# Kernel tuning notes

Hardware: AMD Instinct MI355X
Metric: run time of the kernel (lower is better)

The kernel has to match this reference:

```python
import jax, jax.numpy as jnp
import numpy as np
from jax import lax

SEQ_LEN, PRED_LEN, C_IN, D_MODEL, KS = 96, 48, 7, 128, 5
PAD = (KS - 1) // 2


def setup_inputs() -> dict:
    key = jax.random.key(0)
    ks = jax.random.split(key, 20)
    B = 512
    s = 0.02
    inp = {
        "x_enc": jax.random.normal(ks[0], (B, SEQ_LEN, C_IN), jnp.float32),
        "x_mark": jax.random.randint(ks[1], (B, SEQ_LEN, 4), 0, 7),
        "y_mark": jax.random.randint(ks[2], (B, SEQ_LEN + PRED_LEN, 4), 0, 7),
        # temporal embedding tables
        "hour_emb": jax.random.normal(ks[3], (24, D_MODEL)) * s,
        "weekday_emb": jax.random.normal(ks[4], (7, D_MODEL)) * s,
        "day_emb": jax.random.normal(ks[5], (32, D_MODEL)) * s,
        "month_emb": jax.random.normal(ks[6], (13, D_MODEL)) * s,
        # value embedding Linear(C_IN -> D_MODEL)
        "W_val": jax.random.normal(ks[7], (D_MODEL, C_IN)) * s,
        "b_val": jnp.zeros((D_MODEL,)),
        # three Conv1d(D_MODEL, D_MODEL, KS)
        "conv1_w": jax.random.normal(ks[8], (D_MODEL, D_MODEL, KS)) * s,
        "conv1_b": jnp.zeros((D_MODEL,)),
        "conv2_w": jax.random.normal(ks[9], (D_MODEL, D_MODEL, KS)) * s,
        "conv2_b": jnp.zeros((D_MODEL,)),
        "conv3_w": jax.random.normal(ks[10], (D_MODEL, D_MODEL, KS)) * s,
        "conv3_b": jnp.zeros((D_MODEL,)),
        # GRU (PyTorch layout: 3*D rows ordered [r, z, n])
        "gru_Wi": jax.random.normal(ks[11], (3 * D_MODEL, D_MODEL)) * s,
        "gru_Wh": jax.random.normal(ks[12], (3 * D_MODEL, D_MODEL)) * s,
        "gru_bi": jnp.zeros((3 * D_MODEL,)),
        "gru_bh": jnp.zeros((3 * D_MODEL,)),
        # fc Linear(D_MODEL -> C_IN)
        "fc_w": jax.random.normal(ks[13], (C_IN, D_MODEL)) * s,
        "fc_b": jnp.zeros((C_IN,)),
    }
    return inp


def _conv1d(x, w, b):
    # x: [B, D, T], w: [O, I, K]
    y = lax.conv_general_dilated(x, w, window_strides=(1,), padding=[(PAD, PAD)],
                                 dimension_numbers=("NCH", "OIH", "NCH"))
    return y + b[None, :, None]


def _gru_last(x, Wi, Wh, bi, bh):
    # x: [B, T, D] -> final hidden state [B, D] (PyTorch GRU equations)
    B, T, D = x.shape
    gx = jnp.einsum("btd,gd->btg", x, Wi) + bi  # [B, T, 3D]
    h0 = jnp.zeros((B, D), x.dtype)

    def step(h, gxt):
        gh = h @ Wh.T + bh
        r = jax.nn.sigmoid(gxt[:, :D] + gh[:, :D])
        z = jax.nn.sigmoid(gxt[:, D:2 * D] + gh[:, D:2 * D])
        n = jnp.tanh(gxt[:, 2 * D:] + r * gh[:, 2 * D:])
        return (1.0 - z) * n + z * h, None

    h_last, _ = lax.scan(step, h0, jnp.swapaxes(gx, 0, 1))
    return h_last


def reference(x_enc, x_mark, y_mark,
              hour_emb, weekday_emb, day_emb, month_emb,
              W_val, b_val,
              conv1_w, conv1_b, conv2_w, conv2_b, conv3_w, conv3_b,
              gru_Wi, gru_Wh, gru_bi, gru_bh, fc_w, fc_b):
    B = x_enc.shape[0]
    # temporal embedding for the full y_mark window (pointwise; precompute once)
    temb = (hour_emb[y_mark[:, :, 0]] + weekday_emb[y_mark[:, :, 1]]
            + day_emb[y_mark[:, :, 2]] + month_emb[y_mark[:, :, 3]])  # [B, L, D]

    x_cat = jnp.concatenate([x_enc, jnp.zeros((B, PRED_LEN, C_IN), x_enc.dtype)], axis=1)

    def one_step(x_cat, i):
        xw = lax.dynamic_slice(x_cat, (0, i, 0), (B, SEQ_LEN, C_IN))
        tw = lax.dynamic_slice(temb, (0, i, 0), (B, SEQ_LEN, D_MODEL))
        x = jnp.einsum("btc,dc->btd", xw, W_val) + b_val + tw  # [B, T, D]
        x = jnp.swapaxes(x, 1, 2)  # [B, D, T]
        x = jax.nn.relu(_conv1d(x, conv1_w, conv1_b))
        x = jax.nn.relu(_conv1d(x, conv2_w, conv2_b))
        x = jax.nn.relu(_conv1d(x, conv3_w, conv3_b))
        x = jnp.swapaxes(x, 1, 2)  # [B, T, D]
        h = _gru_last(x, gru_Wi, gru_Wh, gru_bi, gru_bh)  # [B, D]
        pred = h @ fc_w.T + fc_b  # [B, C]
        x_cat = lax.dynamic_update_slice(x_cat, pred[:, None, :], (0, SEQ_LEN + i, 0))
        return x_cat, None

    x_cat, _ = lax.scan(one_step, x_cat, jnp.arange(PRED_LEN))
    return x_cat[:, -PRED_LEN:, :]
```

## Files before the change

kernel.cpp:

```cpp
#include <hip/hip_runtime.h>

#define B_SZ 512
#define SEQ 96
#define PRED 48
#define TOT 144
#define CIN 7
#define DM 128
#define GDIM 384
#define KS 5

#define CSTR 132
#define ASUB (20*CSTR)
#define WROW 136
#define SWZ(o) ((o) + ((((o) >> 6)) << 2))

#define W_CONV (KS*DM*DM)
#define OFF_WIT (3*W_CONV)
#define OFF_WHT (3*W_CONV + DM*GDIM)
#define W_TOTAL (3*W_CONV + 2*DM*GDIM)

#define NBB 2

__device__ float g_gxg[(size_t)B_SZ*TOT*GDIM];
__device__ float g_gxe[B_SZ*12*GDIM];
__device__ float g_wT[W_TOTAL];

__global__ void prep_weights(const float* __restrict__ w1, const float* __restrict__ w2,
                             const float* __restrict__ w3, const float* __restrict__ Wi,
                             const float* __restrict__ Wh) {
    int tid = blockIdx.x*256 + threadIdx.x;
    if (tid < 3*W_CONV) {
        int l = tid / W_CONV, r = tid % W_CONV;
        int o = r & 127, c = (r >> 7) & 127, k = r >> 14;
        const float* w = (l==0) ? w1 : ((l==1) ? w2 : w3);
        g_wT[tid] = w[o*(DM*KS) + c*KS + k];
    } else if (tid < W_TOTAL) {
        int r = tid - 3*W_CONV;
        int m = r / (DM*GDIM), q = r % (DM*GDIM);
        int g = q % GDIM, c = q / GDIM;
        const float* W = (m==0) ? Wi : Wh;
        g_wT[tid] = W[g*DM + c];
    }
}

template<int NJ>
__device__ __forceinline__ void fma8(float (&acc)[NJ][8], int j, float a,
                                     const float4& wA, const float4& wB) {
    acc[j][0] = fmaf(a, wA.x, acc[j][0]);
    acc[j][1] = fmaf(a, wA.y, acc[j][1]);
    acc[j][2] = fmaf(a, wA.z, acc[j][2]);
    acc[j][3] = fmaf(a, wA.w, acc[j][3]);
    acc[j][4] = fmaf(a, wB.x, acc[j][4]);
    acc[j][5] = fmaf(a, wB.y, acc[j][5]);
    acc[j][6] = fmaf(a, wB.z, acc[j][6]);
    acc[j][7] = fmaf(a, wB.w, acc[j][7]);
}

__device__ __forceinline__ void stage_conv_chunk(float* __restrict__ wbuf,
                                                 const float* __restrict__ wT,
                                                 int cc, int tid) {
    const int cj = tid >> 5, oo = (tid & 31) * 4;
    #pragma unroll
    for (int k = 0; k < KS; ++k)
        *(float4*)(wbuf + (k*8 + cj)*WROW + SWZ(oo)) =
            *(const float4*)(wT + (k*DM + cc*8 + cj)*DM + oo);
}

template<int NJ>
__device__ __forceinline__ void conv_layer_chunked(float* __restrict__ buf,
                                                   float* __restrict__ wbuf,
                                                   const float* __restrict__ wT,
                                                   const float* __restrict__ bias,
                                                   int nrow, int winO, int tid) {
    const int og = tid & 15, ttg = tid >> 4;
    const int o0 = og*8, so0 = SWZ(o0), r0 = ttg*NJ;
    const bool act = (r0 < nrow);
    float acc[NJ][8];
// ... 82 lines not shown
    const float* WiT = g_wT + OFF_WIT;
    float ga[3][24];
    #pragma unroll
    for (int e = 0; e < 24; ++e) {
        float bv = gbi[g0+e];
        #pragma unroll
        for (int j = 0; j < 3; ++j) ga[j][e] = bv;
    }
    for (int cc = 0; cc < DM/8; ++cc) {
        __syncthreads();
        #pragma unroll
        for (int s = 0; s < 3; ++s)
            ((float4*)wbuf)[s*256 + tid] = ((const float4*)(WiT + cc*8*GDIM))[s*256 + tid];
        __syncthreads();
        const int c0 = cc*8;
        #pragma unroll
        for (int cj = 0; cj < 8; cj += 2) {
            float2 a2[3];
            #pragma unroll
            for (int m = 0; m < 3; ++m)
                a2[m] = *(const float2*)(buf + (r0+m)*CSTR + c0 + cj);
            float4 w4[6];
            #pragma unroll
            for (int q = 0; q < 6; ++q)
                w4[q] = *(const float4*)(wbuf + cj*GDIM + g0 + q*4);
            const float* wv = (const float*)w4;
            #pragma unroll
            for (int j = 0; j < 3; ++j)
                #pragma unroll
                for (int e = 0; e < 24; ++e)
                    ga[j][e] = fmaf(a2[j].x, wv[e], ga[j][e]);
            #pragma unroll
            for (int q = 0; q < 6; ++q)
                w4[q] = *(const float4*)(wbuf + (cj+1)*GDIM + g0 + q*4);
            #pragma unroll
            for (int j = 0; j < 3; ++j)
                #pragma unroll
                for (int e = 0; e < 24; ++e)
                    ga[j][e] = fmaf(a2[j].y, wv[e], ga[j][e]);
        }
    }
    #pragma unroll
    for (int j = 0; j < 3; ++j) {
        int w = cs + r0 + j;
        if (w >= 6 && w < 90) {
            float* gxo = g_gxg + ((size_t)b*TOT + w)*GDIM + g0;
            #pragma unroll
            for (int q = 0; q < 6; ++q)
                *(float4*)(gxo + q*4) = *(const float4*)&ga[j][q*4];
        }
    }
}

template<int NJ>
__device__ __forceinline__ void mlayer(float* __restrict__ abuf, float* __restrict__ wbuf,
                                       const float* __restrict__ wT,
                                       const float* __restrict__ bias,
                                       int R, int off, int tid) {
    const int og = tid & 15, ttg = tid >> 4;
    const int o0 = og*8, so0 = SWZ(o0);
    const int m0 = ttg * NJ;
    const bool act = (m0 < 2*R);
    int s = 0, r0 = 0;
    if (act) { s = m0 / R; r0 = m0 - s*R; }
    float* in = abuf + s*ASUB;
    float acc[NJ][8];
    #pragma unroll
    for (int u = 0; u < 8; ++u) {
        float bv = bias[o0+u];
        #pragma unroll
        for (int j = 0; j < NJ; ++j) acc[j][u] = bv;
    }
    for (int cc = 0; cc < DM/8; ++cc) {
        __syncthreads();
        stage_conv_chunk(wbuf, wT, cc, tid);
        __syncthreads();
        if (act) {
            const int c0 = cc*8;
            #pragma unroll
            for (int cj = 0; cj < 8; cj += 2) {
                float2 a2[NJ+4];
                #pragma unroll
                for (int m = 0; m < NJ+4; ++m)
                    a2[m] = *(const float2*)(in + (r0+m)*CSTR + c0 + cj);
                #pragma unroll
                for (int k = 0; k < KS; ++k) {
                    const float4 wA0 = *(const float4*)(wbuf + (k*8+cj)*WROW + so0);
                    const float4 wB0 = *(const float4*)(wbuf + (k*8+cj)*WROW + so0 + 4);
                    const float4 wA1 = *(const float4*)(wbuf + (k*8+cj+1)*WROW + so0);
                    const float4 wB1 = *(const float4*)(wbuf + (k*8+cj+1)*WROW + so0 + 4);
                    #pragma unroll
                    for (int j = 0; j < NJ; ++j) {
                        fma8(acc, j, a2[j+k].x, wA0, wB0);
                        fma8(acc, j, a2[j+k].y, wA1, wB1);
                    }
                }
            }
        }
    }
    __syncthreads();
    if (act) {
        const int wb = s ? 83 : -6;
        #pragma unroll
        for (int j = 0; j < NJ; ++j) {
            int q = r0 + j, w = wb + off + q;
            bool valid = (w >= 0) && (w < SEQ);
            #pragma unroll
            for (int u = 0; u < 8; ++u)
                in[q*CSTR + o0+u] = valid ? fmaxf(acc[j][u], 0.f) : 0.f;
        }
    }
    __syncthreads();
}

__launch_bounds__(256, 3)
__global__ void step_kernel(int i, const float* __restrict__ x_enc,
                            const int* __restrict__ y_mark,
                            const float* __restrict__ hour_e, const float* __restrict__ wk_e,
                            const float* __restrict__ day_e, const float* __restrict__ mon_e,
                            const float* __restrict__ W_val, const float* __restrict__ b_val,
                            const float* __restrict__ b1, const float* __restrict__ b2,
                            const float* __restrict__ b3, const float* __restrict__ gbi,
                            const float* __restrict__ out) {
    __shared__ float abuf[2*ASUB];
    __shared__ float wbuf[16*GDIM];
    const int tid = threadIdx.x;
    const int b = blockIdx.x;

    for (int e = tid; e < 2*20*DM; e += 256) {
        int s = e / (20*DM);
        int rem = e - s*(20*DM);
        int q = rem >> 7, d = rem & 127;
        int wb = s ? 83 : -6;
        int w = wb + q;
        float v = 0.f;
        if (w >= 0 && w < SEQ) {
            int p = i + w;
            const float* xr = (p < SEQ) ? (x_enc + (b*SEQ + p)*CIN)
                                        : (out + (b*PRED + (p - SEQ))*CIN);
            v = b_val[d];
            #pragma unroll
            for (int c = 0; c < CIN; ++c) v = fmaf(xr[c], W_val[d*CIN + c], v);
            const int* ym = y_mark + (b*TOT + p)*4;
            v += hour_e[ym[0]*DM + d] + wk_e[ym[1]*DM + d]
               + day_e[ym[2]*DM + d] + mon_e[ym[3]*DM + d];
        }
        abuf[s*ASUB + q*CSTR + d] = v;
    }
    mlayer<2>(abuf, wbuf, g_wT,            b1, 16, 2, tid);
    mlayer<2>(abuf, wbuf, g_wT + W_CONV,   b2, 12, 4, tid);
    mlayer<1>(abuf, wbuf, g_wT + 2*W_CONV, b3,  8, 6, tid);

    const int mp = tid >> 5;
    const int g0 = (tid & 31) * 12;
    const int s = mp >> 2;
    const int row0 = (2*mp) & 7;
    const float* a0p = abuf + s*ASUB + row0*CSTR;
    const float* a1p = a0p + CSTR;
    const float* WiT = g_wT + OFF_WIT;
    float ga[2][12];
    #pragma unroll
    for (int e = 0; e < 12; ++e) { float bv = gbi[g0+e]; ga[0][e] = bv; ga[1][e] = bv; }
    for (int cc = 0; cc < 8; ++cc) {
        __syncthreads();
        for (int x = tid; x < 16*GDIM/4; x += 256)
            ((float4*)wbuf)[x] = ((const float4*)(WiT + cc*16*GDIM))[x];
        __syncthreads();
        #pragma unroll
        for (int c = 0; c < 16; ++c) {
            float av0 = a0p[cc*16 + c];
            float av1 = a1p[cc*16 + c];
            const float* wr = wbuf + c*GDIM + g0;
            #pragma unroll
            for (int q4 = 0; q4 < 3; ++q4) {
                float4 w4 = *(const float4*)(wr + q4*4);
                ga[0][q4*4+0] = fmaf(av0, w4.x, ga[0][q4*4+0]);
                ga[0][q4*4+1] = fmaf(av0, w4.y, ga[0][q4*4+1]);
                ga[0][q4*4+2] = fmaf(av0, w4.z, ga[0][q4*4+2]);
                ga[0][q4*4+3] = fmaf(av0, w4.w, ga[0][q4*4+3]);
                ga[1][q4*4+0] = fmaf(av1, w4.x, ga[1][q4*4+0]);
                ga[1][q4*4+1] = fmaf(av1, w4.y, ga[1][q4*4+1]);
                ga[1][q4*4+2] = fmaf(av1, w4.z, ga[1][q4*4+2]);
                ga[1][q4*4+3] = fmaf(av1, w4.w, ga[1][q4*4+3]);
            }
        }
    }
    const int wb = s ? 83 : -6;
    #pragma unroll
    for (int j = 0; j < 2; ++j) {
        int w = wb + 6 + row0 + j;
        float* dst = nullptr;
        if (s == 0) {
            if (w < 6) dst = g_gxe + ((size_t)b*12 + w)*GDIM + g0;
        } else {
            if (w == 89)      dst = g_gxg + ((size_t)b*TOT + (i + 89))*GDIM + g0;
            else if (w < SEQ) dst = g_gxe + ((size_t)b*12 + (w - 84))*GDIM + g0;
        }
        if (dst) {
            *(float4*)(dst)     = *(const float4*)&ga[j][0];
            *(float4*)(dst + 4) = *(const float4*)&ga[j][4];
            *(float4*)(dst + 8) = *(const float4*)&ga[j][8];
        }
    }
}

__launch_bounds__(512, 2)
__global__ void gru_rec(int i, const float* __restrict__ gbh,
                        const float* __restrict__ fc_w, const float* __restrict__ fc_b,
                        float* __restrict__ out) {
    __shared__ __align__(16) float H[2][NBB][DM];
    __shared__ float P[3][4][NBB][DM];
    const int tid = threadIdx.x;
    const int j = tid & 127, s = tid >> 7;
    const int b0 = blockIdx.x * NBB;

    float whr[32], whz[32], whn[32];
    {
        const float* Wp = g_wT + OFF_WHT + (size_t)(32*s)*GDIM + j;
        #pragma unroll
        for (int c = 0; c < 32; ++c) {
            whr[c] = Wp[c*GDIM];
            whz[c] = Wp[c*GDIM + DM];
            whn[c] = Wp[c*GDIM + 2*DM];
        }
    }

    const int cb = s & 1, cj = j;
    const bool comb = (tid < NBB*DM);
    float bhr = 0.f, bhz = 0.f, bhn = 0.f;
    if (comb) {
        bhr = gbh[cj]; bhz = gbh[DM + cj]; bhn = gbh[2*DM + cj];
        H[0][cb][cj] = 0.f;
    }

    const float* gxg_b0 = g_gxg + (size_t)(b0)*TOT*GDIM;
    const float* gxe_b0 = g_gxe + (size_t)(b0)*12*GDIM;
    auto gp = [&](int t, int bb) -> const float* {
        return (t < 6)  ? (gxe_b0 + (size_t)bb*12*GDIM + t*GDIM)
             : (t < 90) ? (gxg_b0 + (size_t)bb*TOT*GDIM + (size_t)(i + t)*GDIM)
                        : (gxe_b0 + (size_t)bb*12*GDIM + (t - 84)*GDIM);
    };

    float gxr = 0.f, gxz = 0.f, gxn = 0.f;
    if (comb) {
        const float* g0p = gp(0, cb);
        gxr = g0p[cj]; gxz = g0p[DM + cj]; gxn = g0p[2*DM + cj];
    }
    __syncthreads();

    for (int t = 0; t < SEQ; ++t) {
        #pragma unroll
        for (int b = 0; b < NBB; ++b) {
            const float* Hc = &H[t & 1][b][32*s];
            float ar = 0.f, az = 0.f, an = 0.f;
            #pragma unroll
            for (int c = 0; c < 32; c += 4) {
                float4 h4 = *(const float4*)(Hc + c);
                ar = fmaf(h4.x, whr[c],   ar); az = fmaf(h4.x, whz[c],   az); an = fmaf(h4.x, whn[c],   an);
                ar = fmaf(h4.y, whr[c+1], ar); az = fmaf(h4.y, whz[c+1], az); an = fmaf(h4.y, whn[c+1], an);
                ar = fmaf(h4.z, whr[c+2], ar); az = fmaf(h4.z, whz[c+2], az); an = fmaf(h4.z, whn[c+2], an);
                ar = fmaf(h4.w, whr[c+3], ar); az = fmaf(h4.w, whz[c+3], az); an = fmaf(h4.w, whn[c+3], an);
            }
            P[0][s][b][j] = ar;
            P[1][s][b][j] = az;
            P[2][s][b][j] = an;
        }
        __syncthreads();
        if (comb) {
            float ar = bhr + ((P[0][0][cb][cj] + P[0][1][cb][cj]) + (P[0][2][cb][cj] + P[0][3][cb][cj]));
            float az = bhz + ((P[1][0][cb][cj] + P[1][1][cb][cj]) + (P[1][2][cb][cj] + P[1][3][cb][cj]));
            float an = bhn + ((P[2][0][cb][cj] + P[2][1][cb][cj]) + (P[2][2][cb][cj] + P[2][3][cb][cj]));
            float r = 1.f/(1.f + __expf(-(gxr + ar)));
            float z = 1.f/(1.f + __expf(-(gxz + az)));
            float xn = gxn + r*an;
            float e2 = __expf(2.f*xn);
            float n = 1.f - 2.f/(e2 + 1.f);
            float h = (1.f - z)*n + z*H[t & 1][cb][cj];
            H[(t + 1) & 1][cb][cj] = h;
            if (t + 1 < SEQ) {
                const float* gq = gp(t + 1, cb);
                gxr = gq[cj]; gxz = gq[DM + cj]; gxn = gq[2*DM + cj];
            }
        }
        __syncthreads();
    }

    if (tid < NBB*CIN) {
        int bb = tid / CIN, o = tid % CIN;
        float p = fc_b[o];
        const float* Hf = H[0][bb];
        #pragma unroll
        for (int d = 0; d < DM; ++d) p = fmaf(fc_w[o*DM + d], Hf[d], p);
        out[((b0 + bb)*PRED + i)*CIN + o] = p;
    }
}

extern "C" void kernel_launch(void* const* d_in, const int* in_sizes, int n_in,
                              void* d_out, int out_size, void* d_ws, size_t ws_size,
                              hipStream_t stream) {
    const float* x_enc  = (const float*)d_in[0];
    const int*   y_mark = (const int*)d_in[2];
    const float* hour_e = (const float*)d_in[3];
    const float* wk_e   = (const float*)d_in[4];
    const float* day_e  = (const float*)d_in[5];
    const float* mon_e  = (const float*)d_in[6];
    const float* W_val  = (const float*)d_in[7];
    const float* b_val  = (const float*)d_in[8];
    const float* c1w    = (const float*)d_in[9];
    const float* c1b    = (const float*)d_in[10];
    const float* c2w    = (const float*)d_in[11];
    const float* c2b    = (const float*)d_in[12];
    const float* c3w    = (const float*)d_in[13];
    const float* c3b    = (const float*)d_in[14];
    const float* Wi     = (const float*)d_in[15];
    const float* Wh     = (const float*)d_in[16];
    const float* gbi    = (const float*)d_in[17];
    const float* gbh    = (const float*)d_in[18];
    const float* fcw    = (const float*)d_in[19];
    const float* fcb    = (const float*)d_in[20];
    float* out = (float*)d_out;

    prep_weights<<<(W_TOTAL + 255)/256, 256, 0, stream>>>(c1w, c2w, c3w, Wi, Wh);

    init_kernel<<<dim3(B_SZ, 2), 256, 0, stream>>>(x_enc, y_mark,
        hour_e, wk_e, day_e, mon_e, W_val, b_val, c1b, c2b, c3b, gbi);

    for (int i = 0; i < PRED; ++i) {
        step_kernel<<<B_SZ, 256, 0, stream>>>(i, x_enc, y_mark,
            hour_e, wk_e, day_e, mon_e, W_val, b_val, c1b, c2b, c3b, gbi, out);
        gru_rec<<<B_SZ/NBB, 512, 0, stream>>>(i, gbh, fcw, fcb, out);
    }
}
```

Measured before the change: 11.55 ms.

## Fuse per-step conv and GRU kernels into one persistent loop kernel

Replaces the 96 launches (a step_kernel and a gru_rec per prediction step) with a single kernel whose blocks each own two batch rows and loop over all 48 prediction steps. Predictions are kept in shared memory so the next step can read them without a global round trip, and the conv weight staging is shared between the two batch halves of a block. This removes launch overhead and inter-kernel gaps. In exchange, grid parallelism falls to 256 blocks of 512 threads, the GRU Wh registers are reloaded every step, and the block is limited by the larger shared-memory footprint.

```diff
diff --git a/kernel.cpp b/kernel.cpp
--- a/kernel.cpp
+++ b/kernel.cpp
@@ -20,6 +20,13 @@
 #define W_TOTAL (3*W_CONV + 2*DM*GDIM)
 
 #define NBB 2
+
+#define N_PREDH (NBB*PRED*8)
+#define L_ABUF  (N_PREDH)
+#define N_ABUF  (NBB*2*ASUB)
+#define L_WBUF  (L_ABUF + N_ABUF)
+#define N_WBUF  (16*GDIM)
+#define L_TOTAL (L_WBUF + N_WBUF)
 
 __device__ float g_gxg[(size_t)B_SZ*TOT*GDIM];
 __device__ float g_gxe[B_SZ*12*GDIM];
@@ -215,8 +222,8 @@
 __device__ __forceinline__ void mlayer(float* __restrict__ abuf, float* __restrict__ wbuf,
                                        const float* __restrict__ wT,
                                        const float* __restrict__ bias,
-                                       int R, int off, int tid) {
-    const int og = tid & 15, ttg = tid >> 4;
+                                       int R, int off, int t8, bool stager) {
+    const int og = t8 & 15, ttg = t8 >> 4;
     const int o0 = og*8, so0 = SWZ(o0);
     const int m0 = ttg * NJ;
     const bool act = (m0 < 2*R);
@@ -232,7 +239,7 @@
     }
     for (int cc = 0; cc < DM/8; ++cc) {
         __syncthreads();
-        stage_conv_chunk(wbuf, wT, cc, tid);
+        if (stager) stage_conv_chunk(wbuf, wT, cc, t8);
         __syncthreads();
         if (act) {
             const int c0 = cc*8;
@@ -272,185 +279,200 @@
     __syncthreads();
 }
 
-__launch_bounds__(256, 3)
-__global__ void step_kernel(int i, const float* __restrict__ x_enc,
-                            const int* __restrict__ y_mark,
-                            const float* __restrict__ hour_e, const float* __restrict__ wk_e,
-                            const float* __restrict__ day_e, const float* __restrict__ mon_e,
-                            const float* __restrict__ W_val, const float* __restrict__ b_val,
-                            const float* __restrict__ b1, const float* __restrict__ b2,
-                            const float* __restrict__ b3, const float* __restrict__ gbi,
-                            const float* __restrict__ out) {
-    __shared__ float abuf[2*ASUB];
-    __shared__ float wbuf[16*GDIM];
-    const int tid = threadIdx.x;
-    const int b = blockIdx.x;
-
-    for (int e = tid; e < 2*20*DM; e += 256) {
-        int s = e / (20*DM);
-        int rem = e - s*(20*DM);
-        int q = rem >> 7, d = rem & 127;
-        int wb = s ? 83 : -6;
-        int w = wb + q;
-        float v = 0.f;
-        if (w >= 0 && w < SEQ) {
-            int p = i + w;
-            const float* xr = (p < SEQ) ? (x_enc + (b*SEQ + p)*CIN)
-                                        : (out + (b*PRED + (p - SEQ))*CIN);
-            v = b_val[d];
-            #pragma unroll
-            for (int c = 0; c < CIN; ++c) v = fmaf(xr[c], W_val[d*CIN + c], v);
-            const int* ym = y_mark + (b*TOT + p)*4;
-            v += hour_e[ym[0]*DM + d] + wk_e[ym[1]*DM + d]
-               + day_e[ym[2]*DM + d] + mon_e[ym[3]*DM + d];
-        }
-        abuf[s*ASUB + q*CSTR + d] = v;
-    }
-    mlayer<2>(abuf, wbuf, g_wT,            b1, 16, 2, tid);
-    mlayer<2>(abuf, wbuf, g_wT + W_CONV,   b2, 12, 4, tid);
-    mlayer<1>(abuf, wbuf, g_wT + 2*W_CONV, b3,  8, 6, tid);
-
-    const int mp = tid >> 5;
-    const int g0 = (tid & 31) * 12;
-    const int s = mp >> 2;
-    const int row0 = (2*mp) & 7;
-    const float* a0p = abuf + s*ASUB + row0*CSTR;
-    const float* a1p = a0p + CSTR;
-    const float* WiT = g_wT + OFF_WIT;
-    float ga[2][12];
-    #pragma unroll
-    for (int e = 0; e < 12; ++e) { float bv = gbi[g0+e]; ga[0][e] = bv; ga[1][e] = bv; }
-    for (int cc = 0; cc < 8; ++cc) {
-        __syncthreads();
-        for (int x = tid; x < 16*GDIM/4; x += 256)
-            ((float4*)wbuf)[x] = ((const float4*)(WiT + cc*16*GDIM))[x];
-        __syncthreads();
-        #pragma unroll
-        for (int c = 0; c < 16; ++c) {
-            float av0 = a0p[cc*16 + c];
-            float av1 = a1p[cc*16 + c];
-            const float* wr = wbuf + c*GDIM + g0;
-            #pragma unroll
-            for (int q4 = 0; q4 < 3; ++q4) {
-                float4 w4 = *(const float4*)(wr + q4*4);
-                ga[0][q4*4+0] = fmaf(av0, w4.x, ga[0][q4*4+0]);
-                ga[0][q4*4+1] = fmaf(av0, w4.y, ga[0][q4*4+1]);
-                ga[0][q4*4+2] = fmaf(av0, w4.z, ga[0][q4*4+2]);
-                ga[0][q4*4+3] = fmaf(av0, w4.w, ga[0][q4*4+3]);
-                ga[1][q4*4+0] = fmaf(av1, w4.x, ga[1][q4*4+0]);
-                ga[1][q4*4+1] = fmaf(av1, w4.y, ga[1][q4*4+1]);
-                ga[1][q4*4+2] = fmaf(av1, w4.z, ga[1][q4*4+2]);
-                ga[1][q4*4+3] = fmaf(av1, w4.w, ga[1][q4*4+3]);
-            }
-        }
-    }
-    const int wb = s ? 83 : -6;
-    #pragma unroll
-    for (int j = 0; j < 2; ++j) {
-        int w = wb + 6 + row0 + j;
-        float* dst = nullptr;
-        if (s == 0) {
-            if (w < 6) dst = g_gxe + ((size_t)b*12 + w)*GDIM + g0;
-        } else {
-            if (w == 89)      dst = g_gxg + ((size_t)b*TOT + (i + 89))*GDIM + g0;
-            else if (w < SEQ) dst = g_gxe + ((size_t)b*12 + (w - 84))*GDIM + g0;
-        }
-        if (dst) {
-            *(float4*)(dst)     = *(const float4*)&ga[j][0];
-            *(float4*)(dst + 4) = *(const float4*)&ga[j][4];
-            *(float4*)(dst + 8) = *(const float4*)&ga[j][8];
-        }
-    }
-}
-
 __launch_bounds__(512, 2)
-__global__ void gru_rec(int i, const float* __restrict__ gbh,
-                        const float* __restrict__ fc_w, const float* __restrict__ fc_b,
-                        float* __restrict__ out) {
-    __shared__ __align__(16) float H[2][NBB][DM];
-    __shared__ float P[3][4][NBB][DM];
-    const int tid = threadIdx.x;
-    const int j = tid & 127, s = tid >> 7;
-    const int b0 = blockIdx.x * NBB;
-
-    float whr[32], whz[32], whn[32];
-    {
-        const float* Wp = g_wT + OFF_WHT + (size_t)(32*s)*GDIM + j;
-        #pragma unroll
-        for (int c = 0; c < 32; ++c) {
-            whr[c] = Wp[c*GDIM];
-            whz[c] = Wp[c*GDIM + DM];
-            whn[c] = Wp[c*GDIM + 2*DM];
-        }
-    }
-
-    const int cb = s & 1, cj = j;
+__global__ void fused_loop(const float* __restrict__ x_enc,
+                           const int* __restrict__ y_mark,
+                           const float* __restrict__ hour_e, const float* __restrict__ wk_e,
+                           const float* __restrict__ day_e, const float* __restrict__ mon_e,
+                           const float* __restrict__ W_val, const float* __restrict__ b_val,
+                           const float* __restrict__ b1, const float* __restrict__ b2,
+                           const float* __restrict__ b3, const float* __restrict__ gbi,
+                           const float* __restrict__ gbh,
+                           const float* __restrict__ fc_w, const float* __restrict__ fc_b,
+                           float* __restrict__ out) {
+    __shared__ __align__(16) float lds[L_TOTAL];
+    float* const predH = lds;
+    float* const wbuf  = lds + L_WBUF;
+    float* const Hbuf  = wbuf;
+    float* const Pbuf  = wbuf + 2*NBB*DM;
+
+    const int tid  = threadIdx.x;
+    const int half = tid >> 8;
+    const int t8   = tid & 255;
+    const int b0   = blockIdx.x * NBB;
+    const int b    = b0 + half;
+    float* const ab = lds + L_ABUF + half*(2*ASUB);
+
+    const int gj = tid & 127, sl = tid >> 7;
+    const int cb = sl & 1, cj = gj;
     const bool comb = (tid < NBB*DM);
     float bhr = 0.f, bhz = 0.f, bhn = 0.f;
-    if (comb) {
-        bhr = gbh[cj]; bhz = gbh[DM + cj]; bhn = gbh[2*DM + cj];
-        H[0][cb][cj] = 0.f;
-    }
-
-    const float* gxg_b0 = g_gxg + (size_t)(b0)*TOT*GDIM;
-    const float* gxe_b0 = g_gxe + (size_t)(b0)*12*GDIM;
-    auto gp = [&](int t, int bb) -> const float* {
-        return (t < 6)  ? (gxe_b0 + (size_t)bb*12*GDIM + t*GDIM)
-             : (t < 90) ? (gxg_b0 + (size_t)bb*TOT*GDIM + (size_t)(i + t)*GDIM)
-                        : (gxe_b0 + (size_t)bb*12*GDIM + (t - 84)*GDIM);
-    };
-
-    float gxr = 0.f, gxz = 0.f, gxn = 0.f;
-    if (comb) {
-        const float* g0p = gp(0, cb);
-        gxr = g0p[cj]; gxz = g0p[DM + cj]; gxn = g0p[2*DM + cj];
-    }
-    __syncthreads();
-
-    for (int t = 0; t < SEQ; ++t) {
-        #pragma unroll
-        for (int b = 0; b < NBB; ++b) {
-            const float* Hc = &H[t & 1][b][32*s];
-            float ar = 0.f, az = 0.f, an = 0.f;
-            #pragma unroll
-            for (int c = 0; c < 32; c += 4) {
-                float4 h4 = *(const float4*)(Hc + c);
-                ar = fmaf(h4.x, whr[c],   ar); az = fmaf(h4.x, whz[c],   az); an = fmaf(h4.x, whn[c],   an);
-                ar = fmaf(h4.y, whr[c+1], ar); az = fmaf(h4.y, whz[c+1], az); an = fmaf(h4.y, whn[c+1], an);
-                ar = fmaf(h4.z, whr[c+2], ar); az = fmaf(h4.z, whz[c+2], az); an = fmaf(h4.z, whn[c+2], an);
-                ar = fmaf(h4.w, whr[c+3], ar); az = fmaf(h4.w, whz[c+3], az); an = fmaf(h4.w, whn[c+3], an);
-            }
-            P[0][s][b][j] = ar;
-            P[1][s][b][j] = az;
-            P[2][s][b][j] = an;
-        }
-        __syncthreads();
+    if (comb) { bhr = gbh[cj]; bhz = gbh[DM + cj]; bhn = gbh[2*DM + cj]; }
+
+    const float* gxg_b0 = g_gxg + (size_t)b0*TOT*GDIM;
+    const float* gxe_b0 = g_gxe + (size_t)b0*12*GDIM;
+
+    #pragma unroll 1
+    for (int i = 0; i < PRED; ++i) {
+        __syncthreads();
+
+        for (int e = t8; e < 2*20*DM; e += 256) {
+            int s = e / (20*DM);
+            int rem = e - s*(20*DM);
+            int q = rem >> 7, d = rem & 127;
+            int w = (s ? 83 : -6) + q;
+            float v = 0.f;
+            if (w >= 0 && w < SEQ) {
+                int p = i + w;
+                v = b_val[d];
+                if (p < SEQ) {
+                    const float* xr = x_enc + (b*SEQ + p)*CIN;
+                    #pragma unroll
+                    for (int c = 0; c < CIN; ++c) v = fmaf(xr[c], W_val[d*CIN + c], v);
+                } else {
+                    const float* xr = predH + (half*PRED + (p - SEQ))*8;
+                    #pragma unroll
+                    for (int c = 0; c < CIN; ++c) v = fmaf(xr[c], W_val[d*CIN + c], v);
+                }
+                const int* ym = y_mark + (b*TOT + p)*4;
+                v += hour_e[ym[0]*DM + d] + wk_e[ym[1]*DM + d]
+                   + day_e[ym[2]*DM + d] + mon_e[ym[3]*DM + d];
+            }
+            ab[s*ASUB + q*CSTR + d] = v;
+        }
+        mlayer<2>(ab, wbuf, g_wT,            b1, 16, 2, t8, half == 0);
+        mlayer<2>(ab, wbuf, g_wT + W_CONV,   b2, 12, 4, t8, half == 0);
+        mlayer<1>(ab, wbuf, g_wT + 2*W_CONV, b3,  8, 6, t8, half == 0);
+
+        {
+            const int mp = t8 >> 5;
+            const int g0 = (t8 & 31) * 12;
+            const int ssub = mp >> 2;
+            const int row0 = (2*mp) & 7;
+            const float* a0p = ab + ssub*ASUB + row0*CSTR;
+            const float* a1p = a0p + CSTR;
+            const float* WiT = g_wT + OFF_WIT;
+            float ga[2][12];
+            #pragma unroll
+            for (int e = 0; e < 12; ++e) { float bv = gbi[g0+e]; ga[0][e] = bv; ga[1][e] = bv; }
+            for (int cc = 0; cc < 8; ++cc) {
+                __syncthreads();
+                for (int x = tid; x < 16*GDIM/4; x += 512)
+                    ((float4*)wbuf)[x] = ((const float4*)(WiT + cc*16*GDIM))[x];
+                __syncthreads();
+                #pragma unroll
+                for (int c = 0; c < 16; ++c) {
+                    float av0 = a0p[cc*16 + c];
+                    float av1 = a1p[cc*16 + c];
+                    const float* wr = wbuf + c*GDIM + g0;
+                    #pragma unroll
+                    for (int q4 = 0; q4 < 3; ++q4) {
+                        float4 w4 = *(const float4*)(wr + q4*4);
+                        ga[0][q4*4+0] = fmaf(av0, w4.x, ga[0][q4*4+0]);
+                        ga[0][q4*4+1] = fmaf(av0, w4.y, ga[0][q4*4+1]);
+                        ga[0][q4*4+2] = fmaf(av0, w4.z, ga[0][q4*4+2]);
+                        ga[0][q4*4+3] = fmaf(av0, w4.w, ga[0][q4*4+3]);
+                        ga[1][q4*4+0] = fmaf(av1, w4.x, ga[1][q4*4+0]);
+                        ga[1][q4*4+1] = fmaf(av1, w4.y, ga[1][q4*4+1]);
+                        ga[1][q4*4+2] = fmaf(av1, w4.z, ga[1][q4*4+2]);
+                        ga[1][q4*4+3] = fmaf(av1, w4.w, ga[1][q4*4+3]);
+                    }
+                }
+            }
+            const int wb = ssub ? 83 : -6;
+            #pragma unroll
+            for (int jj = 0; jj < 2; ++jj) {
+                int w = wb + 6 + row0 + jj;
+                float* dst = nullptr;
+                if (ssub == 0) {
+                    if (w < 6) dst = g_gxe + ((size_t)b*12 + w)*GDIM + g0;
+                } else {
+                    if (w == 89)      dst = g_gxg + ((size_t)b*TOT + (i + 89))*GDIM + g0;
+                    else if (w < SEQ) dst = g_gxe + ((size_t)b*12 + (w - 84))*GDIM + g0;
+                }
+                if (dst) {
+                    *(float4*)(dst)     = *(const float4*)&ga[jj][0];
+                    *(float4*)(dst + 4) = *(const float4*)&ga[jj][4];
+                    *(float4*)(dst + 8) = *(const float4*)&ga[jj][8];
+                }
+            }
+        }
+
+        __syncthreads();
+
+        float whr[32], whz[32], whn[32];
+        {
+            const float* Wp = g_wT + OFF_WHT + (size_t)(32*sl)*GDIM + gj;
+            #pragma unroll
+            for (int c = 0; c < 32; ++c) {
+                whr[c] = Wp[c*GDIM];
+                whz[c] = Wp[c*GDIM + DM];
+                whn[c] = Wp[c*GDIM + 2*DM];
+            }
+        }
+        if (comb) Hbuf[cb*DM + cj] = 0.f;
+
+        auto gp = [&](int t, int bb) -> const float* {
+            return (t < 6)  ? (gxe_b0 + (size_t)bb*12*GDIM + t*GDIM)
+                 : (t < 90) ? (gxg_b0 + (size_t)bb*TOT*GDIM + (size_t)(i + t)*GDIM)
+                            : (gxe_b0 + (size_t)bb*12*GDIM + (t - 84)*GDIM);
+        };
+
+        float gxr = 0.f, gxz = 0.f, gxn = 0.f;
         if (comb) {
-            float ar = bhr + ((P[0][0][cb][cj] + P[0][1][cb][cj]) + (P[0][2][cb][cj] + P[0][3][cb][cj]));
-            float az = bhz + ((P[1][0][cb][cj] + P[1][1][cb][cj]) + (P[1][2][cb][cj] + P[1][3][cb][cj]));
-            float an = bhn + ((P[2][0][cb][cj] + P[2][1][cb][cj]) + (P[2][2][cb][cj] + P[2][3][cb][cj]));
-            float r = 1.f/(1.f + __expf(-(gxr + ar)));
-            float z = 1.f/(1.f + __expf(-(gxz + az)));
-            float xn = gxn + r*an;
-            float e2 = __expf(2.f*xn);
-            float n = 1.f - 2.f/(e2 + 1.f);
-            float h = (1.f - z)*n + z*H[t & 1][cb][cj];
-            H[(t + 1) & 1][cb][cj] = h;
-            if (t + 1 < SEQ) {
-                const float* gq = gp(t + 1, cb);
-                gxr = gq[cj]; gxz = gq[DM + cj]; gxn = gq[2*DM + cj];
-            }
-        }
-        __syncthreads();
-    }
-
-    if (tid < NBB*CIN) {
-        int bb = tid / CIN, o = tid % CIN;
-        float p = fc_b[o];
-        const float* Hf = H[0][bb];
-        #pragma unroll
-        for (int d = 0; d < DM; ++d) p = fmaf(fc_w[o*DM + d], Hf[d], p);
-        out[((b0 + bb)*PRED + i)*CIN + o] = p;
+            const float* g0p = gp(0, cb);
+            gxr = g0p[cj]; gxz = g0p[DM + cj]; gxn = g0p[2*DM + cj];
+        }
+        __syncthreads();
+
+        for (int t = 0; t < SEQ; ++t) {
+            #pragma unroll
+            for (int bb = 0; bb < NBB; ++bb) {
+                const float* Hc = Hbuf + ((t & 1)*NBB + bb)*DM + 32*sl;
+                float ar = 0.f, az = 0.f, an = 0.f;
+                #pragma unroll
+                for (int c = 0; c < 32; c += 4) {
+                    float4 h4 = *(const float4*)(Hc + c);
+                    ar = fmaf(h4.x, whr[c],   ar); az = fmaf(h4.x, whz[c],   az); an = fmaf(h4.x, whn[c],   an);
+                    ar = fmaf(h4.y, whr[c+1], ar); az = fmaf(h4.y, whz[c+1], az); an = fmaf(h4.y, whn[c+1], an);
+                    ar = fmaf(h4.z, whr[c+2], ar); az = fmaf(h4.z, whz[c+2], az); an = fmaf(h4.z, whn[c+2], an);
+                    ar = fmaf(h4.w, whr[c+3], ar); az = fmaf(h4.w, whz[c+3], az); an = fmaf(h4.w, whn[c+3], an);
+                }
+                Pbuf[((0*4 + sl)*NBB + bb)*DM + gj] = ar;
+                Pbuf[((1*4 + sl)*NBB + bb)*DM + gj] = az;
+                Pbuf[((2*4 + sl)*NBB + bb)*DM + gj] = an;
+            }
+            __syncthreads();
+            if (comb) {
+                #define PIX(g,s) Pbuf[(((g)*4 + (s))*NBB + cb)*DM + cj]
+                float ar = bhr + ((PIX(0,0) + PIX(0,1)) + (PIX(0,2) + PIX(0,3)));
+                float az = bhz + ((PIX(1,0) + PIX(1,1)) + (PIX(1,2) + PIX(1,3)));
+                float an = bhn + ((PIX(2,0) + PIX(2,1)) + (PIX(2,2) + PIX(2,3)));
+                #undef PIX
+                float r = 1.f/(1.f + __expf(-(gxr + ar)));
+                float z = 1.f/(1.f + __expf(-(gxz + az)));
+                float xn = gxn + r*an;
+                float e2 = __expf(2.f*xn);
+                float n = 1.f - 2.f/(e2 + 1.f);
+                float h = (1.f - z)*n + z*Hbuf[((t & 1)*NBB + cb)*DM + cj];
+                Hbuf[(((t + 1) & 1)*NBB + cb)*DM + cj] = h;
+                if (t + 1 < SEQ) {
+                    const float* gq = gp(t + 1, cb);
+                    gxr = gq[cj]; gxz = gq[DM + cj]; gxn = gq[2*DM + cj];
+                }
+            }
+            __syncthreads();
+        }
+
+        if (tid < NBB*CIN) {
+            int bb = tid / CIN, o = tid % CIN;
+            float p = fc_b[o];
+            const float* Hf = Hbuf + bb*DM;
+            #pragma unroll
+            for (int d = 0; d < DM; ++d) p = fmaf(fc_w[o*DM + d], Hf[d], p);
+            out[((b0 + bb)*PRED + i)*CIN + o] = p;
+            predH[(bb*PRED + i)*8 + o] = p;
+        }
     }
 }
 
@@ -484,9 +506,7 @@
     init_kernel<<<dim3(B_SZ, 2), 256, 0, stream>>>(x_enc, y_mark,
         hour_e, wk_e, day_e, mon_e, W_val, b_val, c1b, c2b, c3b, gbi);
 
-    for (int i = 0; i < PRED; ++i) {
-        step_kernel<<<B_SZ, 256, 0, stream>>>(i, x_enc, y_mark,
-            hour_e, wk_e, day_e, mon_e, W_val, b_val, c1b, c2b, c3b, gbi, out);
-        gru_rec<<<B_SZ/NBB, 512, 0, stream>>>(i, gbh, fcw, fcb, out);
-    }
-}
+    fused_loop<<<B_SZ/NBB, 512, 0, stream>>>(x_enc, y_mark,
+        hour_e, wk_e, day_e, mon_e, W_val, b_val, c1b, c2b, c3b,
+        gbi, gbh, fcw, fcb, out);
+}
```

Result: slower. 16.83 ms (+45.7%).

## Reduce GRU partial sums with wavefront shuffles instead of shared memory

Applied to the files above, without the earlier changes.

The recurrent GRU kernel now maps the four K-slices of each hidden unit onto adjacent lanes and combines them with xor shuffles. This removes the shared-memory partial-sum buffer and one block barrier per timestep, and every thread computes the gate nonlinearities redundantly. The hidden state is kept in registers, and only one lane per group writes it to a padded shared layout (stride 36) to reduce bank conflicts. Gate inputs for the next step are prefetched before the matvec. In exchange, the exp and divide work is repeated four times across lanes.

```diff
diff --git a/kernel.cpp b/kernel.cpp
--- a/kernel.cpp
+++ b/kernel.cpp
@@ -364,18 +364,17 @@
 }
 
 __launch_bounds__(512, 2)
-__global__ void gru_rec(int i, const float* __restrict__ gbh,
-                        const float* __restrict__ fc_w, const float* __restrict__ fc_b,
-                        float* __restrict__ out) {
-    __shared__ __align__(16) float H[2][NBB][DM];
-    __shared__ float P[3][4][NBB][DM];
+__global__ void gru_rec2(int i, const float* __restrict__ gbh,
+                         const float* __restrict__ fc_w, const float* __restrict__ fc_b,
+                         float* __restrict__ out) {
+    __shared__ __align__(16) float H[2][NBB][144];
     const int tid = threadIdx.x;
-    const int j = tid & 127, s = tid >> 7;
+    const int gj4 = tid >> 2, s4 = tid & 3;
     const int b0 = blockIdx.x * NBB;
 
     float whr[32], whz[32], whn[32];
     {
-        const float* Wp = g_wT + OFF_WHT + (size_t)(32*s)*GDIM + j;
+        const float* Wp = g_wT + OFF_WHT + (size_t)(32*s4)*GDIM + gj4;
         #pragma unroll
         for (int c = 0; c < 32; ++c) {
             whr[c] = Wp[c*GDIM];
@@ -383,34 +382,41 @@
             whn[c] = Wp[c*GDIM + 2*DM];
         }
     }
-
-    const int cb = s & 1, cj = j;
-    const bool comb = (tid < NBB*DM);
-    float bhr = 0.f, bhz = 0.f, bhn = 0.f;
-    if (comb) {
-        bhr = gbh[cj]; bhz = gbh[DM + cj]; bhn = gbh[2*DM + cj];
-        H[0][cb][cj] = 0.f;
-    }
-
-    const float* gxg_b0 = g_gxg + (size_t)(b0)*TOT*GDIM;
-    const float* gxe_b0 = g_gxe + (size_t)(b0)*12*GDIM;
+    const float bhr = gbh[gj4], bhz = gbh[DM + gj4], bhn = gbh[2*DM + gj4];
+
+    for (int e = tid; e < 2*NBB*144; e += 512) ((float*)H)[e] = 0.f;
+
+    const float* gxg_b0 = g_gxg + (size_t)b0*TOT*GDIM;
+    const float* gxe_b0 = g_gxe + (size_t)b0*12*GDIM;
     auto gp = [&](int t, int bb) -> const float* {
         return (t < 6)  ? (gxe_b0 + (size_t)bb*12*GDIM + t*GDIM)
              : (t < 90) ? (gxg_b0 + (size_t)bb*TOT*GDIM + (size_t)(i + t)*GDIM)
                         : (gxe_b0 + (size_t)bb*12*GDIM + (t - 84)*GDIM);
     };
 
-    float gxr = 0.f, gxz = 0.f, gxn = 0.f;
-    if (comb) {
-        const float* g0p = gp(0, cb);
-        gxr = g0p[cj]; gxz = g0p[DM + cj]; gxn = g0p[2*DM + cj];
+    float gxr[NBB], gxz[NBB], gxn[NBB], hold[NBB];
+    #pragma unroll
+    for (int bb = 0; bb < NBB; ++bb) {
+        const float* g0p = gp(0, bb);
+        gxr[bb] = g0p[gj4]; gxz[bb] = g0p[DM + gj4]; gxn[bb] = g0p[2*DM + gj4];
+        hold[bb] = 0.f;
     }
     __syncthreads();
 
     for (int t = 0; t < SEQ; ++t) {
-        #pragma unroll
-        for (int b = 0; b < NBB; ++b) {
-            const float* Hc = &H[t & 1][b][32*s];
+        float nr[NBB], nz[NBB], nn[NBB];
+        #pragma unroll
+        for (int bb = 0; bb < NBB; ++bb) { nr[bb] = nz[bb] = nn[bb] = 0.f; }
+        if (t + 1 < SEQ) {
+            #pragma unroll
+            for (int bb = 0; bb < NBB; ++bb) {
+                const float* gq = gp(t + 1, bb);
+                nr[bb] = gq[gj4]; nz[bb] = gq[DM + gj4]; nn[bb] = gq[2*DM + gj4];
+            }
+        }
+        #pragma unroll
+        for (int bb = 0; bb < NBB; ++bb) {
+            const float* Hc = &H[t & 1][bb][36*s4];
             float ar = 0.f, az = 0.f, an = 0.f;
             #pragma unroll
             for (int c = 0; c < 32; c += 4) {
@@ -420,26 +426,19 @@
                 ar = fmaf(h4.z, whr[c+2], ar); az = fmaf(h4.z, whz[c+2], az); an = fmaf(h4.z, whn[c+2], an);
                 ar = fmaf(h4.w, whr[c+3], ar); az = fmaf(h4.w, whz[c+3], az); an = fmaf(h4.w, whn[c+3], an);
             }
-            P[0][s][b][j] = ar;
-            P[1][s][b][j] = az;
-            P[2][s][b][j] = an;
-        }
-        __syncthreads();
-        if (comb) {
-            float ar = bhr + ((P[0][0][cb][cj] + P[0][1][cb][cj]) + (P[0][2][cb][cj] + P[0][3][cb][cj]));
-            float az = bhz + ((P[1][0][cb][cj] + P[1][1][cb][cj]) + (P[1][2][cb][cj] + P[1][3][cb][cj]));
-            float an = bhn + ((P[2][0][cb][cj] + P[2][1][cb][cj]) + (P[2][2][cb][cj] + P[2][3][cb][cj]));
-            float r = 1.f/(1.f + __expf(-(gxr + ar)));
-            float z = 1.f/(1.f + __expf(-(gxz + az)));
-            float xn = gxn + r*an;
+            ar += __shfl_xor(ar, 1); ar += __shfl_xor(ar, 2);
+            az += __shfl_xor(az, 1); az += __shfl_xor(az, 2);
+            an += __shfl_xor(an, 1); an += __shfl_xor(an, 2);
+            float r = 1.f/(1.f + __expf(-(gxr[bb] + bhr + ar)));
+            float z = 1.f/(1.f + __expf(-(gxz[bb] + bhz + az)));
+            float xn = gxn[bb] + r*(bhn + an);
             float e2 = __expf(2.f*xn);
             float n = 1.f - 2.f/(e2 + 1.f);
-            float h = (1.f - z)*n + z*H[t & 1][cb][cj];
-            H[(t + 1) & 1][cb][cj] = h;
-            if (t + 1 < SEQ) {
-                const float* gq = gp(t + 1, cb);
-                gxr = gq[cj]; gxz = gq[DM + cj]; gxn = gq[2*DM + cj];
-            }
+            float h = (1.f - z)*n + z*hold[bb];
+            hold[bb] = h;
+            if (s4 == 0)
+                H[(t + 1) & 1][bb][36*(gj4 >> 5) + (gj4 & 31)] = h;
+            gxr[bb] = nr[bb]; gxz[bb] = nz[bb]; gxn[bb] = nn[bb];
         }
         __syncthreads();
     }
@@ -447,9 +446,9 @@
     if (tid < NBB*CIN) {
         int bb = tid / CIN, o = tid % CIN;
         float p = fc_b[o];
-        const float* Hf = H[0][bb];
-        #pragma unroll
-        for (int d = 0; d < DM; ++d) p = fmaf(fc_w[o*DM + d], Hf[d], p);
+        #pragma unroll
+        for (int d = 0; d < DM; ++d)
+            p = fmaf(fc_w[o*DM + d], H[0][bb][36*(d >> 5) + (d & 31)], p);
         out[((b0 + bb)*PRED + i)*CIN + o] = p;
     }
 }
@@ -487,6 +486,6 @@
     for (int i = 0; i < PRED; ++i) {
         step_kernel<<<B_SZ, 256, 0, stream>>>(i, x_enc, y_mark,
             hour_e, wk_e, day_e, mon_e, W_val, b_val, c1b, c2b, c3b, gbi, out);
-        gru_rec<<<B_SZ/NBB, 512, 0, stream>>>(i, gbh, fcw, fcb, out);
-    }
-}
+        gru_rec2<<<B_SZ/NBB, 512, 0, stream>>>(i, gbh, fcw, fcb, out);
+    }
+}
```

After: 12.81 ms. 10.9% more time.

## Precompute left-edge conv/GRU inputs for all steps upfront, keep only right edge per step

Applied to the files above, without the earlier changes.

The left-edge window of each autoregressive step depends only on x_enc, so it is now computed for all 48 steps in one large initL_kernel launch before the loop. Each per-step kernel then only recomputes the right-edge sub-window, which halves its conv work and lets it use a simpler single-row mlayer. The cost is a big upfront parallel kernel and extra global storage for the per-step left-edge gate inputs.

```diff
diff --git a/kernel.cpp b/kernel.cpp
--- a/kernel.cpp
+++ b/kernel.cpp
@@ -22,7 +22,8 @@
 #define NBB 2
 
 __device__ float g_gxg[(size_t)B_SZ*TOT*GDIM];
-__device__ float g_gxe[B_SZ*12*GDIM];
+__device__ float g_gxl[(size_t)B_SZ*PRED*6*GDIM];
+__device__ float g_gxr[(size_t)B_SZ*6*GDIM];
 __device__ float g_wT[W_TOTAL];
 
 __global__ void prep_weights(const float* __restrict__ w1, const float* __restrict__ w2,
@@ -211,25 +212,17 @@
     }
 }
 
-template<int NJ>
-__device__ __forceinline__ void mlayer(float* __restrict__ abuf, float* __restrict__ wbuf,
-                                       const float* __restrict__ wT,
-                                       const float* __restrict__ bias,
-                                       int R, int off, int tid) {
+__device__ __forceinline__ void mlayerR(float* __restrict__ abuf, float* __restrict__ wbuf,
+                                        const float* __restrict__ wT,
+                                        const float* __restrict__ bias,
+                                        int R, int off, int wb, int tid) {
     const int og = tid & 15, ttg = tid >> 4;
     const int o0 = og*8, so0 = SWZ(o0);
-    const int m0 = ttg * NJ;
-    const bool act = (m0 < 2*R);
-    int s = 0, r0 = 0;
-    if (act) { s = m0 / R; r0 = m0 - s*R; }
-    float* in = abuf + s*ASUB;
-    float acc[NJ][8];
+    const int r0 = ttg;
+    const bool act = (r0 < R);
+    float acc[1][8];
     #pragma unroll
-    for (int u = 0; u < 8; ++u) {
-        float bv = bias[o0+u];
-        #pragma unroll
-        for (int j = 0; j < NJ; ++j) acc[j][u] = bv;
-    }
+    for (int u = 0; u < 8; ++u) acc[0][u] = bias[o0+u];
     for (int cc = 0; cc < DM/8; ++cc) {
         __syncthreads();
         stage_conv_chunk(wbuf, wT, cc, tid);
@@ -238,62 +231,128 @@
             const int c0 = cc*8;
             #pragma unroll
             for (int cj = 0; cj < 8; cj += 2) {
-                float2 a2[NJ+4];
+                float2 a2[5];
                 #pragma unroll
-                for (int m = 0; m < NJ+4; ++m)
-                    a2[m] = *(const float2*)(in + (r0+m)*CSTR + c0 + cj);
+                for (int m = 0; m < 5; ++m)
+                    a2[m] = *(const float2*)(abuf + (r0+m)*CSTR + c0 + cj);
                 #pragma unroll
                 for (int k = 0; k < KS; ++k) {
                     const float4 wA0 = *(const float4*)(wbuf + (k*8+cj)*WROW + so0);
                     const float4 wB0 = *(const float4*)(wbuf + (k*8+cj)*WROW + so0 + 4);
                     const float4 wA1 = *(const float4*)(wbuf + (k*8+cj+1)*WROW + so0);
                     const float4 wB1 = *(const float4*)(wbuf + (k*8+cj+1)*WROW + so0 + 4);
-                    #pragma unroll
-                    for (int j = 0; j < NJ; ++j) {
-                        fma8(acc, j, a2[j+k].x, wA0, wB0);
-                        fma8(acc, j, a2[j+k].y, wA1, wB1);
-                    }
+                    fma8(acc, 0, a2[k].x, wA0, wB0);
+                    fma8(acc, 0, a2[k].y, wA1, wB1);
                 }
             }
         }
     }
     __syncthreads();
     if (act) {
-        const int wb = s ? 83 : -6;
-        #pragma unroll
-        for (int j = 0; j < NJ; ++j) {
-            int q = r0 + j, w = wb + off + q;
-            bool valid = (w >= 0) && (w < SEQ);
-            #pragma unroll
-            for (int u = 0; u < 8; ++u)
-                in[q*CSTR + o0+u] = valid ? fmaxf(acc[j][u], 0.f) : 0.f;
-        }
+        int w = wb + off + r0;
+        bool valid = (w >= 0) && (w < SEQ);
+        #pragma unroll
+        for (int u = 0; u < 8; ++u)
+            abuf[r0*CSTR + o0+u] = valid ? fmaxf(acc[0][u], 0.f) : 0.f;
     }
     __syncthreads();
 }
 
+__device__ __forceinline__ void gx_edge(const float* __restrict__ abuf,
+                                        float* __restrict__ wbuf,
+                                        const float* __restrict__ gbi,
+                                        int tid, float (&ga)[12]) {
+    const int row = tid >> 5;
+    const int g0 = (tid & 31) * 12;
+    const float* a0p = abuf + row*CSTR;
+    const float* WiT = g_wT + OFF_WIT;
+    #pragma unroll
+    for (int e = 0; e < 12; ++e) ga[e] = gbi[g0+e];
+    for (int cc = 0; cc < 8; ++cc) {
+        __syncthreads();
+        for (int x = tid; x < 16*GDIM/4; x += 256)
+            ((float4*)wbuf)[x] = ((const float4*)(WiT + cc*16*GDIM))[x];
+        __syncthreads();
+        #pragma unroll
+        for (int c = 0; c < 16; ++c) {
+            float av = a0p[cc*16 + c];
+            const float* wr = wbuf + c*GDIM + g0;
+            #pragma unroll
+            for (int q4 = 0; q4 < 3; ++q4) {
+                float4 w4 = *(const float4*)(wr + q4*4);
+                ga[q4*4+0] = fmaf(av, w4.x, ga[q4*4+0]);
+                ga[q4*4+1] = fmaf(av, w4.y, ga[q4*4+1]);
+                ga[q4*4+2] = fmaf(av, w4.z, ga[q4*4+2]);
+                ga[q4*4+3] = fmaf(av, w4.w, ga[q4*4+3]);
+            }
+        }
+    }
+}
+
 __launch_bounds__(256, 3)
-__global__ void step_kernel(int i, const float* __restrict__ x_enc,
-                            const int* __restrict__ y_mark,
-                            const float* __restrict__ hour_e, const float* __restrict__ wk_e,
-                            const float* __restrict__ day_e, const float* __restrict__ mon_e,
-                            const float* __restrict__ W_val, const float* __restrict__ b_val,
-                            const float* __restrict__ b1, const float* __restrict__ b2,
-                            const float* __restrict__ b3, const float* __restrict__ gbi,
-                            const float* __restrict__ out) {
-    __shared__ float abuf[2*ASUB];
+__global__ void initL_kernel(const float* __restrict__ x_enc,
+                             const int* __restrict__ y_mark,
+                             const float* __restrict__ hour_e, const float* __restrict__ wk_e,
+                             const float* __restrict__ day_e, const float* __restrict__ mon_e,
+                             const float* __restrict__ W_val, const float* __restrict__ b_val,
+                             const float* __restrict__ b1, const float* __restrict__ b2,
+                             const float* __restrict__ b3, const float* __restrict__ gbi) {
+    __shared__ float abuf[ASUB];
     __shared__ float wbuf[16*GDIM];
     const int tid = threadIdx.x;
     const int b = blockIdx.x;
-
-    for (int e = tid; e < 2*20*DM; e += 256) {
-        int s = e / (20*DM);
-        int rem = e - s*(20*DM);
-        int q = rem >> 7, d = rem & 127;
-        int wb = s ? 83 : -6;
-        int w = wb + q;
+    const int kk = blockIdx.y;
+
+    for (int e = tid; e < 20*DM; e += 256) {
+        int q = e >> 7, d = e & 127;
+        int w = -6 + q;
         float v = 0.f;
-        if (w >= 0 && w < SEQ) {
+        if (w >= 0) {
+            int p = kk + w;
+            const float* xr = x_enc + (b*SEQ + p)*CIN;
+            v = b_val[d];
+            #pragma unroll
+            for (int c = 0; c < CIN; ++c) v = fmaf(xr[c], W_val[d*CIN + c], v);
+            const int* ym = y_mark + (b*TOT + p)*4;
+            v += hour_e[ym[0]*DM + d] + wk_e[ym[1]*DM + d]
+               + day_e[ym[2]*DM + d] + mon_e[ym[3]*DM + d];
+        }
+        abuf[q*CSTR + d] = v;
+    }
+    mlayerR(abuf, wbuf, g_wT,            b1, 16, 2, -6, tid);
+    mlayerR(abuf, wbuf, g_wT + W_CONV,   b2, 12, 4, -6, tid);
+    mlayerR(abuf, wbuf, g_wT + 2*W_CONV, b3,  8, 6, -6, tid);
+
+    float ga[12];
+    gx_edge(abuf, wbuf, gbi, tid, ga);
+    const int row = tid >> 5, g0 = (tid & 31) * 12;
+    if (row < 6) {
+        float* dst = g_gxl + (((size_t)b*PRED + kk)*6 + row)*GDIM + g0;
+        *(float4*)(dst)     = *(const float4*)&ga[0];
+        *(float4*)(dst + 4) = *(const float4*)&ga[4];
+        *(float4*)(dst + 8) = *(const float4*)&ga[8];
+    }
+}
+
+__launch_bounds__(256, 3)
+__global__ void stepR_kernel(int i, const float* __restrict__ x_enc,
+                             const int* __restrict__ y_mark,
+                             const float* __restrict__ hour_e, const float* __restrict__ wk_e,
+                             const float* __restrict__ day_e, const float* __restrict__ mon_e,
+                             const float* __restrict__ W_val, const float* __restrict__ b_val,
+                             const float* __restrict__ b1, const float* __restrict__ b2,
+                             const float* __restrict__ b3, const float* __restrict__ gbi,
+                             const float* __restrict__ out) {
+    __shared__ float abuf[ASUB];
+    __shared__ float wbuf[16*GDIM];
+    const int tid = threadIdx.x;
+    const int b = blockIdx.x;
+
+    for (int e = tid; e < 20*DM; e += 256) {
+        int q = e >> 7, d = e & 127;
+        int w = 83 + q;
+        float v = 0.f;
+        if (w < SEQ) {
             int p = i + w;
             const float* xr = (p < SEQ) ? (x_enc + (b*SEQ + p)*CIN)
                                         : (out + (b*PRED + (p - SEQ))*CIN);
@@ -304,62 +363,22 @@
             v += hour_e[ym[0]*DM + d] + wk_e[ym[1]*DM + d]
                + day_e[ym[2]*DM + d] + mon_e[ym[3]*DM + d];
         }
-        abuf[s*ASUB + q*CSTR + d] = v;
-    }
-    mlayer<2>(abuf, wbuf, g_wT,            b1, 16, 2, tid);
-    mlayer<2>(abuf, wbuf, g_wT + W_CONV,   b2, 12, 4, tid);
-    mlayer<1>(abuf, wbuf, g_wT + 2*W_CONV, b3,  8, 6, tid);
-
-    const int mp = tid >> 5;
-    const int g0 = (tid & 31) * 12;
-    const int s = mp >> 2;
-    const int row0 = (2*mp) & 7;
-    const float* a0p = abuf + s*ASUB + row0*CSTR;
-    const float* a1p = a0p + CSTR;
-    const float* WiT = g_wT + OFF_WIT;
-    float ga[2][12];
-    #pragma unroll
-    for (int e = 0; e < 12; ++e) { float bv = gbi[g0+e]; ga[0][e] = bv; ga[1][e] = bv; }
-    for (int cc = 0; cc < 8; ++cc) {
-        __syncthreads();
-        for (int x = tid; x < 16*GDIM/4; x += 256)
-            ((float4*)wbuf)[x] = ((const float4*)(WiT + cc*16*GDIM))[x];
-        __syncthreads();
-        #pragma unroll
-        for (int c = 0; c < 16; ++c) {
-            float av0 = a0p[cc*16 + c];
-            float av1 = a1p[cc*16 + c];
-            const float* wr = wbuf + c*GDIM + g0;
-            #pragma unroll
-            for (int q4 = 0; q4 < 3; ++q4) {
-                float4 w4 = *(const float4*)(wr + q4*4);
-                ga[0][q4*4+0] = fmaf(av0, w4.x, ga[0][q4*4+0]);
-                ga[0][q4*4+1] = fmaf(av0, w4.y, ga[0][q4*4+1]);
-                ga[0][q4*4+2] = fmaf(av0, w4.z, ga[0][q4*4+2]);
-                ga[0][q4*4+3] = fmaf(av0, w4.w, ga[0][q4*4+3]);
-                ga[1][q4*4+0] = fmaf(av1, w4.x, ga[1][q4*4+0]);
-                ga[1][q4*4+1] = fmaf(av1, w4.y, ga[1][q4*4+1]);
-                ga[1][q4*4+2] = fmaf(av1, w4.z, ga[1][q4*4+2]);
-                ga[1][q4*4+3] = fmaf(av1, w4.w, ga[1][q4*4+3]);
-            }
-        }
-    }
-    const int wb = s ? 83 : -6;
-    #pragma unroll
-    for (int j = 0; j < 2; ++j) {
-        int w = wb + 6 + row0 + j;
-        float* dst = nullptr;
-        if (s == 0) {
-            if (w < 6) dst = g_gxe + ((size_t)b*12 + w)*GDIM + g0;
-        } else {
-            if (w == 89)      dst = g_gxg + ((size_t)b*TOT + (i + 89))*GDIM + g0;
-            else if (w < SEQ) dst = g_gxe + ((size_t)b*12 + (w - 84))*GDIM + g0;
-        }
-        if (dst) {
-            *(float4*)(dst)     = *(const float4*)&ga[j][0];
-            *(float4*)(dst + 4) = *(const float4*)&ga[j][4];
-            *(float4*)(dst + 8) = *(const float4*)&ga[j][8];
-        }
+        abuf[q*CSTR + d] = v;
+    }
+    mlayerR(abuf, wbuf, g_wT,            b1, 16, 2, 83, tid);
+    mlayerR(abuf, wbuf, g_wT + W_CONV,   b2, 12, 4, 83, tid);
+    mlayerR(abuf, wbuf, g_wT + 2*W_CONV, b3,  8, 6, 83, tid);
+
+    float ga[12];
+    gx_edge(abuf, wbuf, gbi, tid, ga);
+    const int row = tid >> 5, g0 = (tid & 31) * 12;
+    float* dst = nullptr;
+    if (row == 0)            dst = g_gxg + ((size_t)b*TOT + (i + 89))*GDIM + g0;
+    else if (89 + row < SEQ) dst = g_gxr + ((size_t)b*6 + (row - 1))*GDIM + g0;
+    if (dst) {
+        *(float4*)(dst)     = *(const float4*)&ga[0];
+        *(float4*)(dst + 4) = *(const float4*)&ga[4];
+        *(float4*)(dst + 8) = *(const float4*)&ga[8];
     }
 }
 
@@ -392,12 +411,10 @@
         H[0][cb][cj] = 0.f;
     }
 
-    const float* gxg_b0 = g_gxg + (size_t)(b0)*TOT*GDIM;
-    const float* gxe_b0 = g_gxe + (size_t)(b0)*12*GDIM;
     auto gp = [&](int t, int bb) -> const float* {
-        return (t < 6)  ? (gxe_b0 + (size_t)bb*12*GDIM + t*GDIM)
-             : (t < 90) ? (gxg_b0 + (size_t)bb*TOT*GDIM + (size_t)(i + t)*GDIM)
-                        : (gxe_b0 + (size_t)bb*12*GDIM + (t - 84)*GDIM);
+        return (t < 6)  ? (g_gxl + (((size_t)(b0+bb)*PRED + i)*6 + t)*GDIM)
+             : (t < 90) ? (g_gxg + ((size_t)(b0+bb)*TOT + (i + t))*GDIM)
+                        : (g_gxr + ((size_t)(b0+bb)*6 + (t - 90))*GDIM);
     };
 
     float gxr = 0.f, gxz = 0.f, gxn = 0.f;
@@ -484,8 +501,11 @@
     init_kernel<<<dim3(B_SZ, 2), 256, 0, stream>>>(x_enc, y_mark,
         hour_e, wk_e, day_e, mon_e, W_val, b_val, c1b, c2b, c3b, gbi);
 
+    initL_kernel<<<dim3(B_SZ, PRED), 256, 0, stream>>>(x_enc, y_mark,
+        hour_e, wk_e, day_e, mon_e, W_val, b_val, c1b, c2b, c3b, gbi);
+
     for (int i = 0; i < PRED; ++i) {
-        step_kernel<<<B_SZ, 256, 0, stream>>>(i, x_enc, y_mark,
+        stepR_kernel<<<B_SZ, 256, 0, stream>>>(i, x_enc, y_mark,
             hour_e, wk_e, day_e, mon_e, W_val, b_val, c1b, c2b, c3b, gbi, out);
         gru_rec<<<B_SZ/NBB, 512, 0, stream>>>(i, gbh, fcw, fcb, out);
     }
```

After: 14.26 ms. +23.5%, slower.
